# Performance work log

Hardware: AMD Instinct MI355X
Metric: run time of the kernel (lower is better)

Reference implementation:

```python
import jax, jax.numpy as jnp
import numpy as np

BATCH, SEQ, DIM, NH = 4, 2048, 1024, 16
HD = DIM // NH  # 64

def _rope_cos_sin(seq_len, head_dim, dtype=jnp.float32):
    inv_freq = 1.0 / (10000.0 ** (jnp.arange(0, head_dim, 2, dtype=dtype) / head_dim))
    t = jnp.arange(seq_len, dtype=dtype)
    freqs = jnp.outer(t, inv_freq)                # (seq, hd/2)
    emb = jnp.concatenate([freqs, freqs], axis=-1)  # (seq, hd)
    return jnp.cos(emb), jnp.sin(emb)

def _apply_rope(x, cos, sin):
    # x: (b, h, s, d); cos/sin: (s, d)
    d2 = x.shape[-1] // 2
    x1, x2 = x[..., :d2], x[..., d2:]
    c = cos[None, None, :, :d2]
    s = sin[None, None, :, :d2]
    return jnp.concatenate([x1 * c - x2 * s, x1 * s + x2 * c], axis=-1)

def setup_inputs() -> dict:
    key = jax.random.key(0)
    ks = jax.random.split(key, 3)
    x = jax.random.normal(ks[0], (BATCH, SEQ, DIM), dtype=jnp.float32)
    Wqkv = jax.random.normal(ks[1], (DIM, 3 * DIM), dtype=jnp.float32) * (1.0 / np.sqrt(DIM))
    bqkv = jnp.zeros((3 * DIM,), dtype=jnp.float32)
    Wout = jax.random.normal(ks[2], (DIM, DIM), dtype=jnp.float32) * (1.0 / np.sqrt(DIM))
    bout = jnp.zeros((DIM,), dtype=jnp.float32)
    return {"x": x, "Wqkv": Wqkv, "bqkv": bqkv, "Wout": Wout, "bout": bout}

def reference(x, Wqkv, bqkv, Wout, bout):
    b, s, dim = x.shape
    qkv = x @ Wqkv + bqkv                          # (b, s, 3*dim)
    qkv = qkv.reshape(b, s, 3, NH, HD).transpose(2, 0, 3, 1, 4)  # (3, b, h, s, hd)
    q, k, v = qkv[0], qkv[1], qkv[2]
    cos, sin = _rope_cos_sin(s, HD, x.dtype)
    q = _apply_rope(q, cos, sin)
    k = _apply_rope(k, cos, sin)
    scale = HD ** -0.5
    scores = jnp.einsum('bhqd,bhkd->bhqk', q, k) * scale
    attn = jax.nn.softmax(scores, axis=-1)
    attn = jnp.nan_to_num(attn, nan=0.0)
    out = jnp.einsum('bhqk,bhkd->bhqd', attn, v)   # (b, h, s, hd)
    out = out.transpose(0, 2, 1, 3).reshape(b, s, dim)
    return out @ Wout + bout
```

## Files before the change

kernel.cpp:

```cpp
#include <hip/hip_runtime.h>
#include <hip/hip_bf16.h>
#include <stdint.h>

#define DEVI __device__ __forceinline__

typedef __attribute__((ext_vector_type(8))) short bf16x8;
typedef __attribute__((ext_vector_type(4))) float f32x4;

DEVI float bf2f(short u) {
  union { unsigned int i; float f; } v;
  v.i = ((unsigned int)(unsigned short)u) << 16;
  return v.f;
}
DEVI short f2bf(float f) {
  union { float f; unsigned int i; } v; v.f = f;
  unsigned int r = v.i + 0x7FFFu + ((v.i >> 16) & 1u);
  return (short)(r >> 16);
}

DEVI bf16x8 ldsfrag(const short* t, int row, int k0) {
  int slot = k0 >> 3;
  return *(const bf16x8*)(t + row * 64 + ((slot ^ (row & 7)) << 3));
}

DEVI void gload16(const void* g, void* l) {
  __builtin_amdgcn_global_load_lds((const __attribute__((address_space(1))) void*)g,
                                   (__attribute__((address_space(3))) void*)l, 16, 0, 0);
}

__global__ void k_cvt(const float* __restrict__ in, short* __restrict__ out, int n4) {
  int i = blockIdx.x * blockDim.x + threadIdx.x;
  if (i >= n4) return;
  float4 v = ((const float4*)in)[i];
  short4 o;
  o.x = f2bf(v.x); o.y = f2bf(v.y); o.z = f2bf(v.z); o.w = f2bf(v.w);
  ((short4*)out)[i] = o;
}

__global__ void k_transpose_bf16(const float* __restrict__ in, short* __restrict__ outp,
                                 int R, int C) {
  __shared__ float tile[32][33];
  const int c0 = blockIdx.x * 32, r0 = blockIdx.y * 32;
  const int tx = threadIdx.x, ty = threadIdx.y;
  for (int i = ty; i < 32; i += 8) tile[i][tx] = in[(size_t)(r0 + i) * C + c0 + tx];
  __syncthreads();
  for (int i = ty; i < 32; i += 8) outp[(size_t)(c0 + i) * R + r0 + tx] = f2bf(tile[tx][i]);
}

__global__ void k_rope(float* __restrict__ cosT, float* __restrict__ sinT) {
  int idx = blockIdx.x * blockDim.x + threadIdx.x;
  int s = idx >> 5, i = idx & 31;
  float inv = exp2f(-0.41524101186092034f * (float)i);
  float freq = (float)s * inv;
  cosT[idx] = cosf(freq);
  sinT[idx] = sinf(freq);
}

template <int OUTF32>
__global__ __launch_bounds__(256) void k_gemm(const short* __restrict__ A,
                                              const short* __restrict__ BT,
                                              const float* __restrict__ bias,
                                              void* __restrict__ outp,
                                              int M, int N, int K) {
  __shared__ __align__(16) short As[128 * 64];
  __shared__ __align__(16) short Bs[128 * 64];
  const int tid = threadIdx.x;
  const int lane = tid & 63, wid = tid >> 6;
  const int ln = lane & 15, grp = lane >> 4;
  const int wm = wid >> 1, wn = wid & 1;
  const int r0 = blockIdx.y * 128, c0 = blockIdx.x * 128;

  const short* aSrc[4];
  const short* bSrc[4];
  int ldst[4];
#pragma unroll
  for (int j = 0; j < 4; ++j) {
    int chunk = wid * 256 + j * 64 + lane;
    int row = chunk >> 3, gs = (chunk & 7) ^ (row & 7);
    aSrc[j] = A + (size_t)(r0 + row) * K + gs * 8;
    bSrc[j] = BT + (size_t)(c0 + row) * K + gs * 8;
    ldst[j] = (wid * 256 + j * 64) * 8;
  }

  f32x4 acc[4][4];
#pragma unroll
  for (int i = 0; i < 4; ++i)
#pragma unroll
    for (int j = 0; j < 4; ++j) acc[i][j] = (f32x4){0.f, 0.f, 0.f, 0.f};

  const int nkt = K >> 6;
  for (int kt = 0; kt < nkt; ++kt) {
    __syncthreads();
#pragma unroll
    for (int j = 0; j < 4; ++j) {
      gload16(aSrc[j], &As[ldst[j]]);
      gload16(bSrc[j], &Bs[ldst[j]]);
      aSrc[j] += 64;
      bSrc[j] += 64;
    }
    __syncthreads();
#pragma unroll
    for (int ks = 0; ks < 2; ++ks) {
      const int k0 = ks * 32 + grp * 8;
      bf16x8 af[4], bfr[4];
#pragma unroll
      for (int mi = 0; mi < 4; ++mi) af[mi] = ldsfrag(As, wm * 64 + mi * 16 + ln, k0);
#pragma unroll
      for (int ni = 0; ni < 4; ++ni) bfr[ni] = ldsfrag(Bs, wn * 64 + ni * 16 + ln, k0);
#pragma unroll
      for (int mi = 0; mi < 4; ++mi)
#pragma unroll
        for (int ni = 0; ni < 4; ++ni)
          acc[mi][ni] = __builtin_amdgcn_mfma_f32_16x16x32_bf16(af[mi], bfr[ni], acc[mi][ni], 0, 0, 0);
    }
  }
#pragma unroll
  for (int ni = 0; ni < 4; ++ni) {
    const int col = c0 + wn * 64 + ni * 16 + ln;
    const float bv = bias[col];
#pragma unroll
    for (int mi = 0; mi < 4; ++mi) {
#pragma unroll
      for (int r = 0; r < 4; ++r) {
        const int rowg = r0 + wm * 64 + mi * 16 + grp * 4 + r;
        float v = acc[mi][ni][r] + bv;
        if (OUTF32) ((float*)outp)[(size_t)rowg * N + col] = v;
        else        ((short*)outp)[(size_t)rowg * N + col] = f2bf(v);
      }
    }
  }
}

__global__ __launch_bounds__(256) void k_transform(const short* __restrict__ qkv,
                                                   const float* __restrict__ cosT,
                                                   const float* __restrict__ sinT,
                                                   short* __restrict__ qo,
                                                   short* __restrict__ ko,
                                                   short* __restrict__ vp) {
  __shared__ __align__(16) short vs[64 * 72];
  const int st = blockIdx.x, bh = blockIdx.y;
  const int b = bh >> 4, h = bh & 15;
  const int t = threadIdx.x;
  const float QSC = 0.18033688011112042f;
  {
    const int sl = t >> 2, j = t & 3;
    const int s = st * 64 + sl;
    const short* row = qkv + ((size_t)(b * 2048 + s)) * 3072 + h * 64;
    bf16x8 qlo = *(const bf16x8*)(row + j * 8);
    bf16x8 qhi = *(const bf16x8*)(row + 32 + j * 8);
    bf16x8 klo = *(const bf16x8*)(row + 1024 + j * 8);
    bf16x8 khi = *(const bf16x8*)(row + 1056 + j * 8);
    const float* cp = cosT + s * 32 + j * 8;
    const float* sp = sinT + s * 32 + j * 8;
    bf16x8 ql, qh, kl, kh;
#pragma unroll
    for (int e = 0; e < 8; ++e) {
      float c = cp[e], sn = sp[e];
      float a1 = bf2f(qlo[e]), a2 = bf2f(qhi[e]);
      ql[e] = f2bf((a1 * c - a2 * sn) * QSC);
      qh[e] = f2bf((a1 * sn + a2 * c) * QSC);
      float b1 = bf2f(klo[e]), b2 = bf2f(khi[e]);
      kl[e] = f2bf(b1 * c - b2 * sn);
      kh[e] = f2bf(b1 * sn + b2 * c);
    }
    short* qrow = qo + ((size_t)bh * 2048 + s) * 64;
    short* krow = ko + ((size_t)bh * 2048 + s) * 64;
    *(bf16x8*)(qrow + j * 8) = ql;
    *(bf16x8*)(qrow + 32 + j * 8) = qh;
    *(bf16x8*)(krow + j * 8) = kl;
    *(bf16x8*)(krow + 32 + j * 8) = kh;
    bf16x8 v0 = *(const bf16x8*)(row + 2048 + j * 16);
    bf16x8 v1 = *(const bf16x8*)(row + 2048 + j * 16 + 8);
    *(bf16x8*)(&vs[sl * 72 + j * 16]) = v0;
    *(bf16x8*)(&vs[sl * 72 + j * 16 + 8]) = v1;
  }
  __syncthreads();
  {
#pragma unroll
    for (int i = 0; i < 2; ++i) {
      const int cc = t + i * 256;
      const int ks = cc >> 8, mi = (cc >> 6) & 3, grp = (cc >> 4) & 3, ln = cc & 15;
      const int d = mi * 16 + ln;
      bf16x8 o;
#pragma unroll
      for (int e = 0; e < 8; ++e) {
        const int key = 32 * ks + 16 * (e >> 2) + 4 * grp + (e & 3);
        o[e] = vs[key * 72 + d];
      }
      *(bf16x8*)(vp + ((size_t)bh * 32 + st) * 4096 + cc * 8) = o;
    }
  }
}

__global__ __launch_bounds__(256) void k_attn(const short* __restrict__ Q,
                                              const short* __restrict__ Kk,
                                              const short* __restrict__ Vp,
                                              short* __restrict__ out) {
  __shared__ __align__(16) short smem[2 * 8192];
  const int tid = threadIdx.x;
  const int lane = tid & 63, wid = tid >> 6;
  const int ln = lane & 15, grp = lane >> 4;
  const int qt = blockIdx.x, bh = blockIdx.y;
  const int b = bh >> 4, h = bh & 15;

  bf16x8 qf[2][2];
#pragma unroll
  for (int g = 0; g < 2; ++g)
#pragma unroll
    for (int ks = 0; ks < 2; ++ks)
      qf[g][ks] = *(const bf16x8*)(Q + ((size_t)bh * 2048 + qt * 128 + wid * 32 + g * 16 + ln) * 64
                                   + ks * 32 + grp * 8);

  const short* kSrc0;
  const short* kSrc1;
  const short* vSrc0;
  const short* vSrc1;
  int ldk0, ldk1, ldv0, ldv1;
  {
    int c0i = wid * 64 + lane;
    int r0i = c0i >> 3, g0i = (c0i & 7) ^ (r0i & 7);
    kSrc0 = Kk + (size_t)bh * 2048 * 64 + (size_t)r0i * 64 + g0i * 8;
    ldk0 = wid * 512;
    int c1i = 256 + wid * 64 + lane;
    int r1i = c1i >> 3, g1i = (c1i & 7) ^ (r1i & 7);
    kSrc1 = Kk + (size_t)bh * 2048 * 64 + (size_t)r1i * 64 + g1i * 8;
    ldk1 = 2048 + wid * 512;
    const short* vt = Vp + (size_t)bh * 32 * 4096;
    vSrc0 = vt + (size_t)c0i * 8;
    ldv0 = 4096 + wid * 512;
    vSrc1 = vt + (size_t)c1i * 8;
    ldv1 = 4096 + 2048 + wid * 512;
  }

  f32x4 acc[2][4];
  f32x4 accl[2];
#pragma unroll
  for (int g = 0; g < 2; ++g) {
    accl[g] = (f32x4){0.f, 0.f, 0.f, 0.f};
#pragma unroll
    for (int i = 0; i < 4; ++i) acc[g][i] = (f32x4){0.f, 0.f, 0.f, 0.f};
  }
  bf16x8 ones;
#pragma unroll
  for (int e = 0; e < 8; ++e) ones[e] = (short)0x3F80;

  union PU { bf16x8 v; unsigned int u[4]; };

  gload16(kSrc0, &smem[ldk0]);
  gload16(kSrc1, &smem[ldk1]);
  gload16(vSrc0, &smem[ldv0]);
  gload16(vSrc1, &smem[ldv1]);
  kSrc0 += 4096; kSrc1 += 4096; vSrc0 += 4096; vSrc1 += 4096;
  __syncthreads();

  int cur = 0;
  for (int t = 0; t < 32; ++t) {
    if (t < 31) {
      const int bo = (cur ^ 1) * 8192;
      gload16(kSrc0, &smem[bo + ldk0]);
      gload16(kSrc1, &smem[bo + ldk1]);
      gload16(vSrc0, &smem[bo + ldv0]);
      gload16(vSrc1, &smem[bo + ldv1]);
      kSrc0 += 4096; kSrc1 += 4096; vSrc0 += 4096; vSrc1 += 4096;
    }
    const short* Kb = smem + cur * 8192;
    const short* Vb = Kb + 4096;

    f32x4 sf[2][4];
#pragma unroll
    for (int g = 0; g < 2; ++g)
#pragma unroll
      for (int ni = 0; ni < 4; ++ni) sf[g][ni] = (f32x4){0.f, 0.f, 0.f, 0.f};
#pragma unroll
    for (int ks = 0; ks < 2; ++ks) {
      bf16x8 kf[4];
#pragma unroll
      for (int ni = 0; ni < 4; ++ni) kf[ni] = ldsfrag(Kb, ni * 16 + ln, ks * 32 + grp * 8);
      __builtin_amdgcn_s_setprio(1);
#pragma unroll
      for (int g = 0; g < 2; ++g)
#pragma unroll
        for (int ni = 0; ni < 4; ++ni)
          sf[g][ni] = __builtin_amdgcn_mfma_f32_16x16x32_bf16(kf[ni], qf[g][ks], sf[g][ni], 0, 0, 0);
      __builtin_amdgcn_s_setprio(0);
    }

    PU pbf[2][2];
#pragma unroll
    for (int g = 0; g < 2; ++g) {
#pragma unroll
      for (int ni = 0; ni < 4; ++ni) {
        f32x4 s = sf[g][ni];
#pragma unroll
        for (int r = 0; r < 4; ++r) s[r] = __builtin_amdgcn_exp2f(s[r]);
        sf[g][ni] = s;
      }
#pragma unroll
      for (int ks = 0; ks < 2; ++ks)
#pragma unroll
        for (int j = 0; j < 4; ++j) {
          float lo = sf[g][2 * ks + (j >> 1)][(j & 1) * 2];
          float hi = sf[g][2 * ks + (j >> 1)][(j & 1) * 2 + 1];
          unsigned int r;
          asm("v_cvt_pk_bf16_f32 %0, %1, %2" : "=v"(r) : "v"(lo), "v"(hi));
          pbf[g][ks].u[j] = r;
        }
    }

#pragma unroll
    for (int ks = 0; ks < 2; ++ks) {
      bf16x8 vf[4];
#pragma unroll
      for (int mi = 0; mi < 4; ++mi)
        vf[mi] = *(const bf16x8*)(Vb + (ks * 256 + mi * 64 + lane) * 8);
      __builtin_amdgcn_s_setprio(1);
#pragma unroll
      for (int g = 0; g < 2; ++g) {
#pragma unroll
        for (int mi = 0; mi < 4; ++mi)
          acc[g][mi] = __builtin_amdgcn_mfma_f32_16x16x32_bf16(vf[mi], pbf[g][ks].v, acc[g][mi], 0, 0, 0);
        accl[g] = __builtin_amdgcn_mfma_f32_16x16x32_bf16(ones, pbf[g][ks].v, accl[g], 0, 0, 0);
      }
      __builtin_amdgcn_s_setprio(0);
    }

    __syncthreads();
    cur ^= 1;
  }

#pragma unroll
  for (int g = 0; g < 2; ++g) {
    const float inv = 1.0f / accl[g][0];
    const int q = wid * 32 + g * 16 + ln;
#pragma unroll
    for (int mi = 0; mi < 4; ++mi) {
      short4 p;
      p.x = f2bf(acc[g][mi][0] * inv);
      p.y = f2bf(acc[g][mi][1] * inv);
      p.z = f2bf(acc[g][mi][2] * inv);
      p.w = f2bf(acc[g][mi][3] * inv);
      int slot = mi * 2 + (grp >> 1);
      *(short4*)(&smem[q * 64 + ((slot ^ (q & 7)) << 3) + (grp & 1) * 4]) = p;
    }
  }
  __syncthreads();
  {
    const int row = tid >> 1, half = tid & 1;
#pragma unroll
    for (int j = 0; j < 4; ++j) {
      int c = half * 4 + j;
      int4 v = *(const int4*)(&smem[row * 64 + ((c ^ (row & 7)) << 3)]);
      *(int4*)(out + ((size_t)b * 2048 + qt * 128 + row) * 1024 + h * 64 + c * 8) = v;
    }
  }
}

extern "C" void kernel_launch(void* const* d_in, const int* in_sizes, int n_in,
                              void* d_out, int out_size, void* d_ws, size_t ws_size,
                              hipStream_t stream) {
  const float* x    = (const float*)d_in[0];
  const float* Wqkv = (const float*)d_in[1];
  const float* bqkv = (const float*)d_in[2];
  const float* Wout = (const float*)d_in[3];
  const float* bout = (const float*)d_in[4];
  float* out = (float*)d_out;

  char* p = (char*)d_ws;
  short* xb    = (short*)p; p += (size_t)8192 * 1024 * 2;
  short* wqkvT = (short*)p; p += (size_t)3072 * 1024 * 2;
  short* woutT = (short*)p; p += (size_t)1024 * 1024 * 2;
  float* cosT  = (float*)p; p += (size_t)2048 * 32 * 4;
  float* sinT  = (float*)p; p += (size_t)2048 * 32 * 4;
  short* qkvb  = (short*)p; p += (size_t)8192 * 3072 * 2;
  short* qb    = (short*)p; p += (size_t)64 * 2048 * 64 * 2;
  short* kb    = (short*)p; p += (size_t)64 * 2048 * 64 * 2;
  short* vpb   = (short*)p; p += (size_t)64 * 2048 * 64 * 2;
  short* ao    = (short*)p; p += (size_t)8192 * 1024 * 2;

  k_cvt<<<8192 * 1024 / 4 / 256, 256, 0, stream>>>(x, xb, 8192 * 1024 / 4);
  k_transpose_bf16<<<dim3(3072 / 32, 1024 / 32), dim3(32, 8), 0, stream>>>(Wqkv, wqkvT, 1024, 3072);
  k_transpose_bf16<<<dim3(1024 / 32, 1024 / 32), dim3(32, 8), 0, stream>>>(Wout, woutT, 1024, 1024);
  k_rope<<<2048 * 32 / 256, 256, 0, stream>>>(cosT, sinT);
  k_gemm<0><<<dim3(3072 / 128, 8192 / 128), 256, 0, stream>>>(xb, wqkvT, bqkv, (void*)qkvb,
                                                              8192, 3072, 1024);
  k_transform<<<dim3(32, 64), 256, 0, stream>>>(qkvb, cosT, sinT, qb, kb, vpb);
  k_attn<<<dim3(16, 64), 256, 0, stream>>>(qb, kb, vpb, ao);
  k_gemm<1><<<dim3(1024 / 128, 8192 / 128), 256, 0, stream>>>(ao, woutT, bout, (void*)out,
                                                              8192, 1024, 1024);
}
```

Before: 217.9 us.

## Fuse RoPE, Q scaling and V repacking into the QKV GEMM epilogue

Removes the separate transform kernel and the intermediate bf16 QKV buffer. The QKV GEMM epilogue now applies bias, RoPE and the Q scale, and writes Q, K and pre-permuted V directly through a shared-memory staging tile. The cos/sin table is transposed so each lane can load four consecutive sequence positions with one vector load. This saves a kernel launch and a full write and reread of the QKV tensor, at the cost of a heavier epilogue with an extra LDS round trip. The inline-asm bf16 pack in attention is also swapped for the library intrinsic.

Result: no change. 213.7 us (-1.9%).

```diff
diff --git a/kernel.cpp b/kernel.cpp
--- a/kernel.cpp
+++ b/kernel.cpp
@@ -47,21 +47,150 @@
   for (int i = ty; i < 32; i += 8) outp[(size_t)(c0 + i) * R + r0 + tx] = f2bf(tile[tx][i]);
 }
 
-__global__ void k_rope(float* __restrict__ cosT, float* __restrict__ sinT) {
+__global__ void k_rope(float* __restrict__ cosTt, float* __restrict__ sinTt) {
   int idx = blockIdx.x * blockDim.x + threadIdx.x;
-  int s = idx >> 5, i = idx & 31;
+  int i = idx >> 11, s = idx & 2047;
   float inv = exp2f(-0.41524101186092034f * (float)i);
-  float freq = (float)s * inv;
-  cosT[idx] = cosf(freq);
-  sinT[idx] = sinf(freq);
-}
-
-template <int OUTF32>
-__global__ __launch_bounds__(256) void k_gemm(const short* __restrict__ A,
-                                              const short* __restrict__ BT,
-                                              const float* __restrict__ bias,
-                                              void* __restrict__ outp,
-                                              int M, int N, int K) {
+  float f = (float)s * inv;
+  cosTt[idx] = cosf(f);
+  sinTt[idx] = sinf(f);
+}
+
+__global__ __launch_bounds__(256) void k_gemm_qkv(const short* __restrict__ A,
+                                                  const short* __restrict__ BT,
+                                                  const float* __restrict__ bias,
+                                                  const float* __restrict__ cosTt,
+                                                  const float* __restrict__ sinTt,
+                                                  short* __restrict__ qo,
+                                                  short* __restrict__ ko,
+                                                  short* __restrict__ vp) {
+  __shared__ __align__(16) short smem[17408];
+  short* As = smem;
+  short* Bs = smem + 8192;
+  const int tid = threadIdx.x;
+  const int lane = tid & 63, wid = tid >> 6;
+  const int ln = lane & 15, grp = lane >> 4;
+  const int wm = wid >> 1, wn = wid & 1;
+  const int bx = blockIdx.x;
+  const int r0 = blockIdx.y * 128, c0 = bx * 128;
+  const int K = 1024;
+
+  const short* aSrc[4];
+  const short* bSrc[4];
+  int ldst[4];
+#pragma unroll
+  for (int j = 0; j < 4; ++j) {
+    int chunk = wid * 256 + j * 64 + lane;
+    int row = chunk >> 3, gs = (chunk & 7) ^ (row & 7);
+    aSrc[j] = A + (size_t)(r0 + row) * K + gs * 8;
+    bSrc[j] = BT + (size_t)(c0 + row) * K + gs * 8;
+    ldst[j] = (wid * 256 + j * 64) * 8;
+  }
+
+  f32x4 acc[4][4];
+#pragma unroll
+  for (int i = 0; i < 4; ++i)
+#pragma unroll
+    for (int j = 0; j < 4; ++j) acc[i][j] = (f32x4){0.f, 0.f, 0.f, 0.f};
+
+  for (int kt = 0; kt < 16; ++kt) {
+    __syncthreads();
+#pragma unroll
+    for (int j = 0; j < 4; ++j) {
+      gload16(aSrc[j], &As[ldst[j]]);
+      gload16(bSrc[j], &Bs[ldst[j]]);
+      aSrc[j] += 64;
+      bSrc[j] += 64;
+    }
+    __syncthreads();
+#pragma unroll
+    for (int ks = 0; ks < 2; ++ks) {
+      const int k0 = ks * 32 + grp * 8;
+      bf16x8 af[4], bfr[4];
+#pragma unroll
+      for (int mi = 0; mi < 4; ++mi) af[mi] = ldsfrag(As, wm * 64 + mi * 16 + ln, k0);
+#pragma unroll
+      for (int ni = 0; ni < 4; ++ni) bfr[ni] = ldsfrag(Bs, wn * 64 + ni * 16 + ln, k0);
+#pragma unroll
+      for (int mi = 0; mi < 4; ++mi)
+#pragma unroll
+        for (int ni = 0; ni < 4; ++ni)
+          acc[mi][ni] = __builtin_amdgcn_mfma_f32_16x16x32_bf16(af[mi], bfr[ni], acc[mi][ni], 0, 0, 0);
+    }
+  }
+
+  __syncthreads();
+  const int third = bx >> 3;
+  const int h0 = (bx & 7) * 2;
+  const int b = r0 >> 11, sb = r0 & 2047;
+
+  if (third < 2) {
+    const float QS = (third == 0) ? 0.18033688011112042f : 1.0f;
+#pragma unroll
+    for (int mi = 0; mi < 4; ++mi) {
+      const int s0 = sb + wm * 64 + mi * 16 + grp * 4;
+      const int rowb = (wm * 64 + mi * 16 + grp * 4) * 136 + wn * 64;
+#pragma unroll
+      for (int ni = 0; ni < 2; ++ni) {
+        const int d1 = ni * 16 + ln;
+        float4 cv = *(const float4*)(cosTt + d1 * 2048 + s0);
+        float4 sv = *(const float4*)(sinTt + d1 * 2048 + s0);
+        const float b1 = bias[c0 + wn * 64 + d1];
+        const float b2 = bias[c0 + wn * 64 + d1 + 32];
+#pragma unroll
+        for (int r = 0; r < 4; ++r) {
+          float x1 = acc[mi][ni][r] + b1;
+          float x2 = acc[mi][ni + 2][r] + b2;
+          float c = ((const float*)&cv)[r], s = ((const float*)&sv)[r];
+          smem[rowb + r * 136 + d1]      = f2bf((x1 * c - x2 * s) * QS);
+          smem[rowb + r * 136 + d1 + 32] = f2bf((x1 * s + x2 * c) * QS);
+        }
+      }
+    }
+    __syncthreads();
+    const int rloc = tid >> 1, ph = tid & 1;
+    const int bh = b * 16 + h0 + ph;
+    short* dst = (third == 0 ? qo : ko) + ((size_t)bh * 2048 + sb + rloc) * 64;
+    const short* src = smem + rloc * 136 + ph * 64;
+#pragma unroll
+    for (int j = 0; j < 8; ++j) *(int4*)(dst + j * 8) = *(const int4*)(src + j * 8);
+  } else {
+#pragma unroll
+    for (int mi = 0; mi < 4; ++mi) {
+      const int rowb = (wm * 64 + mi * 16 + grp * 4) * 136 + wn * 64;
+#pragma unroll
+      for (int ni = 0; ni < 4; ++ni) {
+        const float bv = bias[c0 + wn * 64 + ni * 16 + ln];
+#pragma unroll
+        for (int r = 0; r < 4; ++r)
+          smem[rowb + r * 136 + ni * 16 + ln] = f2bf(acc[mi][ni][r] + bv);
+      }
+    }
+    __syncthreads();
+#pragma unroll
+    for (int i = 0; i < 8; ++i) {
+      const int g = i * 256 + tid;
+      const int ph = g >> 10, tt = (g >> 9) & 1, cc2 = g & 511;
+      const int ks = cc2 >> 8, mi = (cc2 >> 6) & 3, grp_ = (cc2 >> 4) & 3, ln_ = cc2 & 15;
+      const int d = mi * 16 + ln_;
+      bf16x8 o;
+#pragma unroll
+      for (int e = 0; e < 8; ++e) {
+        const int key = tt * 64 + 32 * ks + 16 * (e >> 2) + 4 * grp_ + (e & 3);
+        o[e] = smem[key * 136 + ph * 64 + d];
+      }
+      const int bh = b * 16 + h0 + ph;
+      const int tg = (sb >> 6) + tt;
+      *(bf16x8*)(vp + ((size_t)bh * 32 + tg) * 4096 + cc2 * 8) = o;
+    }
+  }
+}
+
+__global__ __launch_bounds__(256) void k_gemm_out(const short* __restrict__ A,
+                                                  const short* __restrict__ BT,
+                                                  const float* __restrict__ bias,
+                                                  float* __restrict__ outp,
+                                                  int M, int N, int K) {
   __shared__ __align__(16) short As[128 * 64];
   __shared__ __align__(16) short Bs[128 * 64];
   const int tid = threadIdx.x;
@@ -123,71 +252,8 @@
 #pragma unroll
       for (int r = 0; r < 4; ++r) {
         const int rowg = r0 + wm * 64 + mi * 16 + grp * 4 + r;
-        float v = acc[mi][ni][r] + bv;
-        if (OUTF32) ((float*)outp)[(size_t)rowg * N + col] = v;
-        else        ((short*)outp)[(size_t)rowg * N + col] = f2bf(v);
-      }
-    }
-  }
-}
-
-__global__ __launch_bounds__(256) void k_transform(const short* __restrict__ qkv,
-                                                   const float* __restrict__ cosT,
-                                                   const float* __restrict__ sinT,
-                                                   short* __restrict__ qo,
-                                                   short* __restrict__ ko,
-                                                   short* __restrict__ vp) {
-  __shared__ __align__(16) short vs[64 * 72];
-  const int st = blockIdx.x, bh = blockIdx.y;
-  const int b = bh >> 4, h = bh & 15;
-  const int t = threadIdx.x;
-  const float QSC = 0.18033688011112042f;
-  {
-    const int sl = t >> 2, j = t & 3;
-    const int s = st * 64 + sl;
-    const short* row = qkv + ((size_t)(b * 2048 + s)) * 3072 + h * 64;
-    bf16x8 qlo = *(const bf16x8*)(row + j * 8);
-    bf16x8 qhi = *(const bf16x8*)(row + 32 + j * 8);
-    bf16x8 klo = *(const bf16x8*)(row + 1024 + j * 8);
-    bf16x8 khi = *(const bf16x8*)(row + 1056 + j * 8);
-    const float* cp = cosT + s * 32 + j * 8;
-    const float* sp = sinT + s * 32 + j * 8;
-    bf16x8 ql, qh, kl, kh;
-#pragma unroll
-    for (int e = 0; e < 8; ++e) {
-      float c = cp[e], sn = sp[e];
-      float a1 = bf2f(qlo[e]), a2 = bf2f(qhi[e]);
-      ql[e] = f2bf((a1 * c - a2 * sn) * QSC);
-      qh[e] = f2bf((a1 * sn + a2 * c) * QSC);
-      float b1 = bf2f(klo[e]), b2 = bf2f(khi[e]);
-      kl[e] = f2bf(b1 * c - b2 * sn);
-      kh[e] = f2bf(b1 * sn + b2 * c);
-    }
-    short* qrow = qo + ((size_t)bh * 2048 + s) * 64;
-    short* krow = ko + ((size_t)bh * 2048 + s) * 64;
-    *(bf16x8*)(qrow + j * 8) = ql;
-    *(bf16x8*)(qrow + 32 + j * 8) = qh;
-    *(bf16x8*)(krow + j * 8) = kl;
-    *(bf16x8*)(krow + 32 + j * 8) = kh;
-    bf16x8 v0 = *(const bf16x8*)(row + 2048 + j * 16);
-    bf16x8 v1 = *(const bf16x8*)(row + 2048 + j * 16 + 8);
-    *(bf16x8*)(&vs[sl * 72 + j * 16]) = v0;
-    *(bf16x8*)(&vs[sl * 72 + j * 16 + 8]) = v1;
-  }
-  __syncthreads();
-  {
-#pragma unroll
-    for (int i = 0; i < 2; ++i) {
-      const int cc = t + i * 256;
-      const int ks = cc >> 8, mi = (cc >> 6) & 3, grp = (cc >> 4) & 3, ln = cc & 15;
-      const int d = mi * 16 + ln;
-      bf16x8 o;
-#pragma unroll
-      for (int e = 0; e < 8; ++e) {
-        const int key = 32 * ks + 16 * (e >> 2) + 4 * grp + (e & 3);
-        o[e] = vs[key * 72 + d];
-      }
-      *(bf16x8*)(vp + ((size_t)bh * 32 + st) * 4096 + cc * 8) = o;
+        outp[(size_t)rowg * N + col] = acc[mi][ni][r] + bv;
+      }
     }
   }
 }
@@ -245,6 +311,7 @@
   for (int e = 0; e < 8; ++e) ones[e] = (short)0x3F80;
 
   union PU { bf16x8 v; unsigned int u[4]; };
+  union CV { __hip_bfloat162 h; unsigned int u; };
 
   gload16(kSrc0, &smem[ldk0]);
   gload16(kSrc1, &smem[ldk1]);
@@ -299,11 +366,10 @@
       for (int ks = 0; ks < 2; ++ks)
 #pragma unroll
         for (int j = 0; j < 4; ++j) {
-          float lo = sf[g][2 * ks + (j >> 1)][(j & 1) * 2];
-          float hi = sf[g][2 * ks + (j >> 1)][(j & 1) * 2 + 1];
-          unsigned int r;
-          asm("v_cvt_pk_bf16_f32 %0, %1, %2" : "=v"(r) : "v"(lo), "v"(hi));
-          pbf[g][ks].u[j] = r;
+          CV cv;
+          cv.h = __float22bfloat162_rn(make_float2(sf[g][2 * ks + (j >> 1)][(j & 1) * 2],
+                                                   sf[g][2 * ks + (j >> 1)][(j & 1) * 2 + 1]));
+          pbf[g][ks].u[j] = cv.u;
         }
     }
 
@@ -369,9 +435,8 @@
   short* xb    = (short*)p; p += (size_t)8192 * 1024 * 2;
   short* wqkvT = (short*)p; p += (size_t)3072 * 1024 * 2;
   short* woutT = (short*)p; p += (size_t)1024 * 1024 * 2;
-  float* cosT  = (float*)p; p += (size_t)2048 * 32 * 4;
-  float* sinT  = (float*)p; p += (size_t)2048 * 32 * 4;
-  short* qkvb  = (short*)p; p += (size_t)8192 * 3072 * 2;
+  float* cosTt = (float*)p; p += (size_t)32 * 2048 * 4;
+  float* sinTt = (float*)p; p += (size_t)32 * 2048 * 4;
   short* qb    = (short*)p; p += (size_t)64 * 2048 * 64 * 2;
   short* kb    = (short*)p; p += (size_t)64 * 2048 * 64 * 2;
   short* vpb   = (short*)p; p += (size_t)64 * 2048 * 64 * 2;
@@ -380,11 +445,9 @@
   k_cvt<<<8192 * 1024 / 4 / 256, 256, 0, stream>>>(x, xb, 8192 * 1024 / 4);
   k_transpose_bf16<<<dim3(3072 / 32, 1024 / 32), dim3(32, 8), 0, stream>>>(Wqkv, wqkvT, 1024, 3072);
   k_transpose_bf16<<<dim3(1024 / 32, 1024 / 32), dim3(32, 8), 0, stream>>>(Wout, woutT, 1024, 1024);
-  k_rope<<<2048 * 32 / 256, 256, 0, stream>>>(cosT, sinT);
-  k_gemm<0><<<dim3(3072 / 128, 8192 / 128), 256, 0, stream>>>(xb, wqkvT, bqkv, (void*)qkvb,
-                                                              8192, 3072, 1024);
-  k_transform<<<dim3(32, 64), 256, 0, stream>>>(qkvb, cosT, sinT, qb, kb, vpb);
+  k_rope<<<32 * 2048 / 256, 256, 0, stream>>>(cosTt, sinTt);
+  k_gemm_qkv<<<dim3(24, 64), 256, 0, stream>>>(xb, wqkvT, bqkv, cosTt, sinTt, qb, kb, vpb);
   k_attn<<<dim3(16, 64), 256, 0, stream>>>(qb, kb, vpb, ao);
-  k_gemm<1><<<dim3(1024 / 128, 8192 / 128), 256, 0, stream>>>(ao, woutT, bout, (void*)out,
-                                                              8192, 1024, 1024);
-}
+  k_gemm_out<<<dim3(1024 / 128, 8192 / 128), 256, 0, stream>>>(ao, woutT, bout, out,
+                                                               8192, 1024, 1024);
+}
```
